# Kernel tuning notes

Hardware: AMD Instinct MI355X
Metric: run time of the kernel (lower is better)

The kernel has to match this reference:

```python
import jax, jax.numpy as jnp
import numpy as np

B, M, D = 512, 100000, 256
EPS = 1e-8  # torch.cosine_similarity eps
TEMP = 10.0  # softmax temperature from source


def setup_inputs() -> dict:
    key = jax.random.key(0)
    kx, kk, kv = jax.random.split(key, 3)
    x = jax.random.normal(kx, (B, D), dtype=jnp.float32)
    memory_keys = jax.random.normal(kk, (M, D), dtype=jnp.float32) * 0.1
    memory_values = jax.random.normal(kv, (M, D), dtype=jnp.float32) * 0.1
    return {"x": x, "memory_keys": memory_keys, "memory_values": memory_values}


def reference(x, memory_keys, memory_values):
    # cosine similarity between x [B,D] and memory_keys [M,D] -> [B,M]
    dots = jnp.einsum("bd,md->bm", x, memory_keys)
    xn = jnp.linalg.norm(x, axis=-1)          # [B]
    kn = jnp.linalg.norm(memory_keys, axis=-1)  # [M]
    denom = jnp.maximum(xn[:, None] * kn[None, :], EPS)
    sims = dots / denom                         # [B,M]
    attn = jax.nn.softmax(sims * TEMP, axis=-1)  # [B,M]
    retrieved = jnp.einsum("bm,md->bd", attn, memory_values)  # [B,D]
    return retrieved, attn
```

## Files before the change

### kernel.cpp

```cpp
#include <hip/hip_runtime.h>
#include <hip/hip_bf16.h>


#define MCOLS 100000
#define MP    100032
#define DDIM  256
#define CHUNK 1792
#define NTFULL 28
#define NCHUNK 56
#define NSLOT 56
#define CHUNK1 832
#define NT1   26
#define ATTN_OFF 131072
#define WS_RXN  0
#define WS_RKN  512
#define WS_RCPL 100512
#define WS_XB_BYTE   409600ull
#define WS_VT_BYTE   1048576ull
#define WS_PART_BYTE 52264960ull
#define WS_KB_BYTE   84246528ull
#define WS_KB_END    (WS_KB_BYTE + 2ull*(size_t)MCOLS*DDIM)

#define GLL(g, l) __builtin_amdgcn_global_load_lds( \
    (const __attribute__((address_space(1))) void*)(g), \
    (__attribute__((address_space(3))) void*)(l), 16, 0, 0)

typedef short short8 __attribute__((ext_vector_type(8)));
typedef float f32x4  __attribute__((ext_vector_type(4)));

static __device__ __forceinline__ unsigned short f2bfu(float f) {
  union { __hip_bfloat16 h; unsigned short u; } cv;
  cv.h = __float2bfloat16(f);
  return cv.u;
}
static __device__ __forceinline__ unsigned int pk2(float a, float b) {
  return (unsigned int)f2bfu(a) | ((unsigned int)f2bfu(b) << 16);
}
static __device__ __forceinline__ short8 pack8(float4 a, float4 b) {
  short8 r;
  r[0] = (short)f2bfu(a.x); r[1] = (short)f2bfu(a.y);
  r[2] = (short)f2bfu(a.z); r[3] = (short)f2bfu(a.w);
  r[4] = (short)f2bfu(b.x); r[5] = (short)f2bfu(b.y);
  r[6] = (short)f2bfu(b.z); r[7] = (short)f2bfu(b.w);
  return r;
}

__global__ void k0_xn(const float* __restrict__ x, float* __restrict__ ws) {
  const int b = blockIdx.x, t = threadIdx.x;
  const float v = x[b*DDIM + t];
  float s = v*v;
  #pragma unroll
  for (int mk = 1; mk <= 32; mk <<= 1) s += __shfl_xor(s, mk);
  __shared__ float ps[4];
  if ((t & 63) == 0) ps[t >> 6] = s;
  __syncthreads();
  const float tot = ps[0] + ps[1] + ps[2] + ps[3];
  const float r10 = 10.0f / fmaxf(sqrtf(tot), 1e-12f);
  if (t == 0) ws[WS_RXN + b] = r10;
  unsigned short* xbp = (unsigned short*)((char*)ws + WS_XB_BYTE);
  xbp[b*DDIM + t] = f2bfu(v * r10);
}

template<bool WRITEKB>
__global__ __launch_bounds__(256) void k0c_kn(const float* __restrict__ K,
                                              float* __restrict__ ws) {
  const int t = threadIdx.x;
  const int mg = blockIdx.x*64 + (t >> 2);
  const int qq = t & 3;
  if (mg >= MCOLS) return;
  const float* kp = K + (size_t)mg*DDIM + 64*qq;
  float4 buf[16];
  float ss = 0.f;
  #pragma unroll
  for (int j = 0; j < 16; ++j) {
    buf[j] = *(const float4*)(kp + 4*j);
    ss += buf[j].x*buf[j].x + buf[j].y*buf[j].y + buf[j].z*buf[j].z + buf[j].w*buf[j].w;
  }
  ss += __shfl_xor(ss, 1); ss += __shfl_xor(ss, 2);
  const float rk = 1.0f / fmaxf(sqrtf(ss), 1e-12f);
  if (qq == 0) ws[WS_RKN + mg] = rk;
  if (WRITEKB) {
    unsigned int* kb = (unsigned int*)((char*)ws + WS_KB_BYTE);
    #pragma unroll
    for (int j = 0; j < 8; ++j) {
      const float4 a = buf[2*j], b2 = buf[2*j+1];
      uint4 u;
      u.x = pk2(a.x*rk, a.y*rk);  u.y = pk2(a.z*rk, a.w*rk);
      u.z = pk2(b2.x*rk, b2.y*rk); u.w = pk2(b2.z*rk, b2.w*rk);
      const int slot = (8*qq + j) ^ (mg & 7);
      *(uint4*)(kb + (size_t)mg*128 + slot*4) = u;
    }
  }
}

__global__ __launch_bounds__(256) void k0b_tr(const float* __restrict__ V,
                                              float* __restrict__ ws) {
  const int t = threadIdx.x;
  const int m0 = blockIdx.x * 64;
  __shared__ float vt_f[64][261];
  #pragma unroll
  for (int i = 0; i < 4; ++i) {
    const int ml = (t >> 4) + 16*i;
    const int mg = m0 + ml;
    #pragma unroll
    for (int j = 0; j < 4; ++j) {
      const int d = 4*(t & 15) + 64*j;
      float4 v = make_float4(0.f, 0.f, 0.f, 0.f);
      if (mg < MCOLS) v = *(const float4*)(V + (size_t)mg*DDIM + d);
      vt_f[ml][d] = v.x; vt_f[ml][d+1] = v.y; vt_f[ml][d+2] = v.z; vt_f[ml][d+3] = v.w;
    }
  }
  __syncthreads();
  unsigned short* vt = (unsigned short*)((char*)ws + WS_VT_BYTE);
  const int tl = t & 15;
  const int s = tl >> 1, hf = tl & 1;
  const int mq = 8*s + 4*hf;
  #pragma unroll
  for (int it = 0; it < 16; ++it) {
    const int d = (t >> 4) + 16*it;
    uint2 u;
    u.x = pk2(vt_f[mq+0][d], vt_f[mq+1][d]);
    u.y = pk2(vt_f[mq+2][d], vt_f[mq+3][d]);
    const int sp = s ^ (d & 7);
    *(uint2*)(vt + (size_t)d*MP + m0 + sp*8 + 4*hf) = u;
  }
}

static __device__ __forceinline__ void stage_k(const char* __restrict__ kb,
                                               int m0, int w, int l,
                                               unsigned short (*klds)[256]) {
  #pragma unroll
  for (int i = 0; i < 4; ++i) {
    int r = m0 + w*8 + i*2 + (l >> 5);
    r = min(r, MCOLS - 1);
    const char* g = kb + (size_t)r*512 + (l & 31)*16;
    char* dst = (char*)&klds[w*8 + i*2][0];
    GLL(g, dst);
  }
}
static __device__ __forceinline__ void stage_k32(const char* __restrict__ kb,
                                                 int m0, int w, int l,
                                                 unsigned short (*klds)[256]) {
  #pragma unroll
  for (int i = 0; i < 2; ++i) {
    int r = m0 + w*4 + i*2 + (l >> 5);
    r = min(r, MCOLS - 1);
    const char* g = kb + (size_t)r*512 + (l & 31)*16;
    char* dst = (char*)&klds[w*4 + i*2][0];
    GLL(g, dst);
  }
}
static __device__ __forceinline__ void stage_vt(const char* __restrict__ vtb,
                                                int m1, int w, int l,
                                                unsigned short (*vtl)[64]) {
  #pragma unroll
  for (int i = 0; i < 4; ++i) {
    const int d = w*32 + i*8 + (l >> 3);
    const int ms = min(m1 + (l & 7)*8, MP - 8);
    const char* g = vtb + ((size_t)d*MP + ms)*2;
    char* dst = (char*)&vtl[w*32 + i*8][0];
    GLL(g, dst);
  }
}

__global__ __launch_bounds__(512, 4) void k1b_sum(const float* __restrict__ ws,
                                                  float* __restrict__ out) {
  const int bid = blockIdx.x;
  const int xg = bid & 7, i = bid >> 3;
  const int c = xg + 8*(i & 15), rb = i >> 4;
  const int t = threadIdx.x, w = t >> 6, l = t & 63, q = l >> 4, ln = l & 15;
  const int ar = w & 3, h = w >> 2, l7 = ln & 7;
  __shared__ __align__(16) unsigned short klds2[2][32][256];
  const char* kb = (const char*)ws + WS_KB_BYTE;
  const unsigned short* xb = (const unsigned short*)((const char*)ws + WS_XB_BYTE);
  const int R0 = rb*128;

  short8 xf[2][8];
  #pragma unroll
  for (int as = 0; as < 2; ++as) {
    const int row = R0 + 32*ar + 16*as + ln;
    #pragma unroll
    for (int kk = 0; kk < 8; ++kk)
      xf[as][kk] = *(const short8*)(xb + row*DDIM + 32*kk + 8*q);
  }
  float lpr[2][4] = {{0.f,0.f,0.f,0.f},{0.f,0.f,0.f,0.f}};
  const int mbase = c*CHUNK1;
  const int rem = MCOLS - mbase;
  const int nt = rem <= 0 ? 0 : min(NT1, (rem + 31) >> 5);

  if (nt > 0) {
    stage_k32(kb, mbase, w, l, klds2[0]);
    __syncthreads();
    for (int mt = 0; mt < nt; ++mt) {
      const int cur = mt & 1;
      const int m0 = mbase + mt*32;
      if (mt + 1 < nt) stage_k32(kb, m0 + 32, w, l, klds2[cur ^ 1]);
      const char* kbase = (const char*)&klds2[cur][0][0];
      const int row0 = 16*h + ln;
      f32x4 acc[2];
      { f32x4 z = {0.f,0.f,0.f,0.f}; acc[0] = z; acc[1] = z; }
      #pragma unroll
      for (int kk = 0; kk < 8; ++kk) {
        const int sl = ((q + 4*kk) ^ l7) << 4;
        const short8 b0 = *(const short8*)(kbase + row0*512 + sl);
        acc[0] = __builtin_amdgcn_mfma_f32_16x16x32_bf16(xf[0][kk], b0, acc[0], 0,0,0);
        acc[1] = __builtin_amdgcn_mfma_f32_16x16x32_bf16(xf[1][kk], b0, acc[1], 0,0,0);
      }
      const int mr = m0 + row0;
      const bool ok = mr < MCOLS;
      #pragma unroll
      for (int as = 0; as < 2; ++as)
        #pragma unroll
        for (int r = 0; r < 4; ++r)
          lpr[as][r] += ok ? __expf(acc[as][r]) : 0.f;
      __syncthreads();
    }
  }
  #pragma unroll
  for (int as = 0; as < 2; ++as)
    #pragma unroll
    for (int r = 0; r < 4; ++r) {
      float s = lpr[as][r];
      s += __shfl_xor(s, 1); s += __shfl_xor(s, 2);
      s += __shfl_xor(s, 4); s += __shfl_xor(s, 8);
      if (ln == 0)
        out[(size_t)(c*2 + h)*512 + R0 + 32*ar + 16*as + 4*q + r] = s;
    }
}

template<int NSUM>
__global__ void k2_final(const float* __restrict__ out, float* __restrict__ ws) {
  const int b = blockIdx.x, t = threadIdx.x;
  float v = (t < NSUM) ? out[(size_t)t*512 + b] : 0.f;
  #pragma unroll
  for (int mk = 1; mk <= 32; mk <<= 1) v += __shfl_xor(v, mk);
  __shared__ float s2[4];
  if ((t & 63) == 0) s2[t >> 6] = v;
  __syncthreads();
  if (t == 0) ws[WS_RCPL + b] = 1.0f / (s2[0] + s2[1] + s2[2] + s2[3]);
}

__global__ __launch_bounds__(512, 4) void k3a_main(float* __restrict__ ws,
                                                   float* __restrict__ out) {
  const int bid = blockIdx.x;
  const int xg = bid & 7, i = bid >> 3;
  const int c = xg + 8*(i % 7), rb = i / 7;
  const int t = threadIdx.x, w = t >> 6, l = t & 63, q = l >> 4, ln = l & 15;
  const int ar = w & 3, h = w >> 2, l7 = ln & 7;
  __shared__ __align__(16) unsigned short klds[64][256];
  __shared__ __align__(16) unsigned short vtl[256][64];
  __shared__ __align__(16) unsigned short plds[64][64];
  const char* kb  = (const char*)ws + WS_KB_BYTE;
  const char* vtb = (const char*)ws + WS_VT_BYTE;
  const unsigned short* xb = (const unsigned short*)((const char*)ws + WS_XB_BYTE);
  const int R0 = rb*64;

  short8 xf[8];
  {
    const int row = R0 + 16*ar + ln;
    #pragma unroll
    for (int kk = 0; kk < 8; ++kk)
      xf[kk] = *(const short8*)(xb + row*DDIM + 32*kk + 8*q);
  }
  float rlq[4];
  #pragma unroll
  for (int r = 0; r < 4; ++r)
    rlq[r] = ws[WS_RCPL + R0 + 16*ar + 4*q + r];
  f32x4 apv[8];
  #pragma unroll
  for (int dx = 0; dx < 8; ++dx) { f32x4 z = {0.f,0.f,0.f,0.f}; apv[dx] = z; }
  const int d2 = 128*h;
  float* attn = out + ATTN_OFF;
  const int mbase = c*CHUNK;
  const int nt = min(NTFULL, (MCOLS - mbase + 63) >> 6);
  unsigned short* pf = &plds[0][0];

  stage_k(kb, mbase, w, l, klds);
  __syncthreads();

  for (int mt = 0; mt < nt; ++mt) {
    const int m0 = mbase + mt*64;
    stage_vt(vtb, m0, w, l, vtl);
    const int row0 = 32*h + ln;
    f32x4 acc[2];
    { f32x4 z = {0.f,0.f,0.f,0.f}; acc[0] = z; acc[1] = z; }
    #pragma unroll
    for (int kk = 0; kk < 8; ++kk) {
      const int sl = ((q + 4*kk) ^ l7) << 4;
      const short8 b0 = *(const short8*)((const char*)&klds[0][0] + row0*512 + sl);
      const short8 b1 = *(const short8*)((const char*)&klds[0][0] + (row0 + 16)*512 + sl);
      acc[0] = __builtin_amdgcn_mfma_f32_16x16x32_bf16(xf[kk], b0, acc[0], 0,0,0);
      acc[1] = __builtin_amdgcn_mfma_f32_16x16x32_bf16(xf[kk], b1, acc[1], 0,0,0);
    }
    const int mr0 = m0 + row0, mr1 = mr0 + 16;
    const bool ok0 = mr0 < MCOLS, ok1 = mr1 < MCOLS;
    #pragma unroll
    for (int r = 0; r < 4; ++r) {
      const int rowl = 16*ar + 4*q + r;
      const float p0v = ok0 ? __expf(acc[0][r]) : 0.f;
      const float p1v = ok1 ? __expf(acc[1][r]) : 0.f;
      float* arow = attn + (size_t)(R0 + rowl)*MCOLS;
      if (ok0) arow[mr0] = p0v*rlq[r];
      if (ok1) arow[mr1] = p1v*rlq[r];
      const int r7 = rowl & 7;
      pf[rowl*64 + ((((ln>>3) + 4*h    ) ^ r7) << 3) + (ln & 7)] = f2bfu(p0v);
      pf[rowl*64 + ((((ln>>3) + 4*h + 2) ^ r7) << 3) + (ln & 7)] = f2bfu(p1v);
    }
    __syncthreads();
    if (mt + 1 < nt) stage_k(kb, m0 + 64, w, l, klds);
    const int prow = 16*ar + ln;
    const short8 af0 = *(const short8*)(pf + prow*64 + ((q       ^ l7) << 3));
    const short8 af1 = *(const short8*)(pf + prow*64 + (((4 + q) ^ l7) << 3));
    #pragma unroll
    for (int dx = 0; dx < 8; ++dx) {
      const int R = d2 + 16*dx + ln;
      const char* vr = (const char*)&vtl[0][0] + R*128;
      const short8 bv0 = *(const short8*)(vr + ((q       ^ l7) << 4));
      const short8 bv1 = *(const short8*)(vr + (((4 + q) ^ l7) << 4));
      apv[dx] = __builtin_amdgcn_mfma_f32_16x16x32_bf16(af0, bv0, apv[dx], 0,0,0);
      apv[dx] = __builtin_amdgcn_mfma_f32_16x16x32_bf16(af1, bv1, apv[dx], 0,0,0);
    }
    __syncthreads();
  }

  float* part = (float*)((char*)ws + WS_PART_BYTE);
  #pragma unroll
  for (int dx = 0; dx < 8; ++dx)
    #pragma unroll
    for (int r = 0; r < 4; ++r)
      part[((size_t)c*512 + R0 + 16*ar + 4*q + r)*256 + d2 + 16*dx + ln]
        = apv[dx][r]*rlq[r];
}

static __device__ __forceinline__ void load_xf(const float* __restrict__ x,
                                               int brow0, int q, int ln,
                                               short8 xf[2][8]) {
  #pragma unroll
  for (int as = 0; as < 2; ++as) {
    const int row = brow0 + 16*as + ln;
    #pragma unroll
    for (int kk = 0; kk < 8; ++kk) {
      const float* p = x + row*DDIM + 32*kk + 8*q;
      xf[as][kk] = pack8(*(const float4*)p, *(const float4*)(p + 4));
    }
  }
}

__global__ __launch_bounds__(512, 2) void k3b_main(const float* __restrict__ x,
                                                   const float* __restrict__ K,
                                                   float* __restrict__ ws,
                                                   float* __restrict__ out) {
  const int bid = blockIdx.x;
  const int c = bid >> 2, rb = bid & 3;
  const int t = threadIdx.x, w = t >> 6, l = t & 63, q = l >> 4, ln = l & 15;
  const int h = w & 1, rg = w >> 1;
  __shared__ __align__(16) unsigned short plds[2][128][72];
  const int R0 = rb*128;
  short8 xf[2][8];
  const int brow0 = R0 + 32*rg;
  load_xf(x, brow0, q, ln, xf);
  float rxn[2][4];
  #pragma unroll
  for (int as = 0; as < 2; ++as)
    #pragma unroll
    for (int r = 0; r < 4; ++r)
      rxn[as][r] = ws[WS_RXN + brow0 + 16*as + 4*q + r];
  float lpr[2][4] = {{0.f,0.f,0.f,0.f},{0.f,0.f,0.f,0.f}};
  f32x4 apv[2][8];
  #pragma unroll
  for (int bs = 0; bs < 2; ++bs)
    #pragma unroll
    for (int dx = 0; dx < 8; ++dx) { f32x4 z = {0.f,0.f,0.f,0.f}; apv[bs][dx] = z; }
  const int b2 = 32*(w & 3), d2 = 128*(w >> 2);
  const unsigned short* vt = (const unsigned short*)((const char*)ws + WS_VT_BYTE);
  const float* rknw = ws + WS_RKN;
  float* attn = out + ATTN_OFF;
  const int mbase = c*CHUNK;
  const int nt = min(NTFULL, (MCOLS - mbase + 63) >> 6);
  const int l7 = ln & 7;

  for (int mt = 0; mt < nt; ++mt) {
    const int m0 = mbase + mt*64;
    const int mr0 = m0 + 32*h + ln, mr1 = mr0 + 16;
    const int kr0 = min(mr0, MCOLS-1), kr1 = min(mr1, MCOLS-1);
    f32x4 acc[2][2];
    #pragma unroll
    for (int as = 0; as < 2; ++as)
      #pragma unroll
      for (int mm = 0; mm < 2; ++mm) { f32x4 z = {0.f,0.f,0.f,0.f}; acc[as][mm] = z; }
    const float* p0 = K + (size_t)kr0*DDIM + 8*q;
    const float* p1 = K + (size_t)kr1*DDIM + 8*q;
    #pragma unroll
    for (int kk = 0; kk < 8; ++kk) {
      const short8 b0 = pack8(*(const float4*)(p0 + 32*kk), *(const float4*)(p0 + 32*kk + 4));
      const short8 b1 = pack8(*(const float4*)(p1 + 32*kk), *(const float4*)(p1 + 32*kk + 4));
      acc[0][0] = __builtin_amdgcn_mfma_f32_16x16x32_bf16(xf[0][kk], b0, acc[0][0], 0,0,0);
      acc[0][1] = __builtin_amdgcn_mfma_f32_16x16x32_bf16(xf[0][kk], b1, acc[0][1], 0,0,0);
      acc[1][0] = __builtin_amdgcn_mfma_f32_16x16x32_bf16(xf[1][kk], b0, acc[1][0], 0,0,0);
      acc[1][1] = __builtin_amdgcn_mfma_f32_16x16x32_bf16(xf[1][kk], b1, acc[1][1], 0,0,0);
    }
    const float rk0 = rknw[kr0], rk1 = rknw[kr1];
    const bool ok0 = mr0 < MCOLS, ok1 = mr1 < MCOLS;
    #pragma unroll
    for (int as = 0; as < 2; ++as)
      #pragma unroll
      for (int r = 0; r < 4; ++r) {
        const int rowl = 32*rg + 16*as + 4*q + r;
        const float p0v = ok0 ? __expf(acc[as][0][r]*rxn[as][r]*rk0) : 0.f;
        const float p1v = ok1 ? __expf(acc[as][1][r]*rxn[as][r]*rk1) : 0.f;
        float* arow = attn + (size_t)(R0 + rowl)*MCOLS;
        if (ok0) arow[mr0] = p0v;
        if (ok1) arow[mr1] = p1v;
        lpr[as][r] += p0v + p1v;
        plds[mt & 1][rowl][32*h + ln]      = f2bfu(p0v);
        plds[mt & 1][rowl][32*h + 16 + ln] = f2bfu(p1v);
      }
    __syncthreads();
    const unsigned short (*pb)[72] = plds[mt & 1];
    const short8 af00 = *(const short8*)&pb[b2 + ln][8*q];
    const short8 af01 = *(const short8*)&pb[b2 + ln][32 + 8*q];
    const short8 af10 = *(const short8*)&pb[b2 + 16 + ln][8*q];
    const short8 af11 = *(const short8*)&pb[b2 + 16 + ln][32 + 8*q];
    #pragma unroll
    for (int dx = 0; dx < 8; ++dx) {
      const int R = d2 + 16*dx + ln;
      const size_t rbase = (size_t)R*MP + m0;
      const short8 bv0 = *(const short8*)(vt + rbase + ((q     ^ (R & 7)) << 3));
      const short8 bv1 = *(const short8*)(vt + rbase + (((4+q) ^ (R & 7)) << 3));
      apv[0][dx] = __builtin_amdgcn_mfma_f32_16x16x32_bf16(af00, bv0, apv[0][dx], 0,0,0);
      apv[0][dx] = __builtin_amdgcn_mfma_f32_16x16x32_bf16(af01, bv1, apv[0][dx], 0,0,0);
      apv[1][dx] = __builtin_amdgcn_mfma_f32_16x16x32_bf16(af10, bv0, apv[1][dx], 0,0,0);
      apv[1][dx] = __builtin_amdgcn_mfma_f32_16x16x32_bf16(af11, bv1, apv[1][dx], 0,0,0);
    }
  }

  #pragma unroll
  for (int as = 0; as < 2; ++as)
    #pragma unroll
    for (int r = 0; r < 4; ++r) {
      float s = lpr[as][r];
      s += __shfl_xor(s, 1); s += __shfl_xor(s, 2);
      s += __shfl_xor(s, 4); s += __shfl_xor(s, 8);
      if (ln == 0)
        out[(size_t)(c*2 + h)*512 + brow0 + 16*as + 4*q + r] = s;
    }
  float* part = (float*)((char*)ws + WS_PART_BYTE);
  #pragma unroll
  for (int bs = 0; bs < 2; ++bs)
    #pragma unroll
    for (int dx = 0; dx < 8; ++dx)
      #pragma unroll
      for (int r = 0; r < 4; ++r)
        part[((size_t)c*512 + R0 + b2 + 16*bs + 4*q + r)*256 + d2 + 16*dx + ln]
          = apv[bs][dx][r];
}

template<bool NORM>
__global__ void k4_red(const float* __restrict__ ws, float* __restrict__ out) {
  const int b = blockIdx.x, t = threadIdx.x;
  const float* part = (const float*)((const char*)ws + WS_PART_BYTE);
  float acc = 0.f;
  for (int cc = 0; cc < NSLOT; ++cc)
    acc += part[((size_t)cc*512 + b)*256 + t];
  if (!NORM) acc *= ws[WS_RCPL + b];
  out[b*DDIM + t] = acc;
}

__global__ void k5_scale(const float* __restrict__ ws, float* __restrict__ out) {
  const int row = blockIdx.y;
  const int i4 = blockIdx.x*256 + threadIdx.x;
  if (i4 >= MCOLS/4) return;
  const float s = ws[WS_RCPL + row];
  float4* p = (float4*)(out + ATTN_OFF + (size_t)row*MCOLS) + i4;
  float4 v = *p;
  v.x *= s; v.y *= s; v.z *= s; v.w *= s;
  *p = v;
}

extern "C" void kernel_launch(void* const* d_in, const int* in_sizes, int n_in,
                              void* d_out, int out_size, void* d_ws, size_t ws_size,
                              hipStream_t stream) {
  const float* x = (const float*)d_in[0];
  const float* K = (const float*)d_in[1];
  const float* V = (const float*)d_in[2];
  float* out = (float*)d_out;
  float* ws  = (float*)d_ws;
  const bool useKB = ws_size >= WS_KB_END;

  k0_xn<<<512, 256, 0, stream>>>(x, ws);
  if (useKB) k0c_kn<true ><<<1563, 256, 0, stream>>>(K, ws);
  else       k0c_kn<false><<<1563, 256, 0, stream>>>(K, ws);
  k0b_tr<<<MP/64, 256, 0, stream>>>(V, ws);
  if (useKB) {
    k1b_sum<<<512, 512, 0, stream>>>(ws, out);
    k2_final<256><<<512, 256, 0, stream>>>(out, ws);
    k3a_main<<<448, 512, 0, stream>>>(ws, out);
    k4_red<true><<<512, 256, 0, stream>>>(ws, out);
  } else {
    k3b_main<<<224, 512, 0, stream>>>(x, K, ws, out);
    k2_final<112><<<512, 256, 0, stream>>>(out, ws);
    k5_scale<<<dim3((MCOLS/4 + 255)/256, 512), 256, 0, stream>>>(ws, out);
    k4_red<false><<<512, 256, 0, stream>>>(ws, out);
  }
}
```

Measured before the change: 244.5 us.

## Re-tile k3a warp mapping so each K fragment feeds two x-row tiles

Reassigns warps in k3a_main so each warp owns 32 query rows by 16 memory columns in the QK^T stage, reusing one K LDS fragment across two MFMAs. In the PV stage each warp covers 32 rows by 64 output columns, reusing V fragments across two row tiles. The aim is to halve LDS reads per MFMA. The 1/sum scaling of partial outputs moves out of k3a, and the reduction kernel is switched to the variant that applies it. The cost is more registers for the doubled x fragments.

```diff
diff --git a/kernel.cpp b/kernel.cpp
--- a/kernel.cpp
+++ b/kernel.cpp
@@ -243,10 +243,12 @@
 __global__ __launch_bounds__(512, 4) void k3a_main(float* __restrict__ ws,
                                                    float* __restrict__ out) {
   const int bid = blockIdx.x;
-  const int xg = bid & 7, i = bid >> 3;
-  const int c = xg + 8*(i % 7), rb = i / 7;
+  const int xcd = bid & 7, i = bid >> 3;
+  const int c = xcd + 8*(i % 7), rb = i / 7;
   const int t = threadIdx.x, w = t >> 6, l = t & 63, q = l >> 4, ln = l & 15;
-  const int ar = w & 3, h = w >> 2, l7 = ln & 7;
+  const int l7 = ln & 7;
+  const int xg = w >> 2, mh = w & 3;
+  const int pg = w & 1,  dg = w >> 1;
   __shared__ __align__(16) unsigned short klds[64][256];
   __shared__ __align__(16) unsigned short vtl[256][64];
   __shared__ __align__(16) unsigned short plds[64][64];
@@ -255,21 +257,23 @@
   const unsigned short* xb = (const unsigned short*)((const char*)ws + WS_XB_BYTE);
   const int R0 = rb*64;
 
-  short8 xf[8];
-  {
-    const int row = R0 + 16*ar + ln;
+  short8 xf[2][8];
+  #pragma unroll
+  for (int s = 0; s < 2; ++s) {
+    const int row = R0 + 32*xg + 16*s + ln;
     #pragma unroll
     for (int kk = 0; kk < 8; ++kk)
-      xf[kk] = *(const short8*)(xb + row*DDIM + 32*kk + 8*q);
-  }
-  float rlq[4];
-  #pragma unroll
-  for (int r = 0; r < 4; ++r)
-    rlq[r] = ws[WS_RCPL + R0 + 16*ar + 4*q + r];
+      xf[s][kk] = *(const short8*)(xb + row*DDIM + 32*kk + 8*q);
+  }
+  float rlq[2][4];
+  #pragma unroll
+  for (int s = 0; s < 2; ++s)
+    #pragma unroll
+    for (int r = 0; r < 4; ++r)
+      rlq[s][r] = ws[WS_RCPL + R0 + 32*xg + 16*s + 4*q + r];
   f32x4 apv[8];
   #pragma unroll
   for (int dx = 0; dx < 8; ++dx) { f32x4 z = {0.f,0.f,0.f,0.f}; apv[dx] = z; }
-  const int d2 = 128*h;
   float* attn = out + ATTN_OFF;
   const int mbase = c*CHUNK;
   const int nt = min(NTFULL, (MCOLS - mbase + 63) >> 6);
@@ -281,55 +285,60 @@
   for (int mt = 0; mt < nt; ++mt) {
     const int m0 = mbase + mt*64;
     stage_vt(vtb, m0, w, l, vtl);
-    const int row0 = 32*h + ln;
+    const int brow = 16*mh + ln;
     f32x4 acc[2];
     { f32x4 z = {0.f,0.f,0.f,0.f}; acc[0] = z; acc[1] = z; }
     #pragma unroll
     for (int kk = 0; kk < 8; ++kk) {
-      const int sl = ((q + 4*kk) ^ l7) << 4;
-      const short8 b0 = *(const short8*)((const char*)&klds[0][0] + row0*512 + sl);
-      const short8 b1 = *(const short8*)((const char*)&klds[0][0] + (row0 + 16)*512 + sl);
-      acc[0] = __builtin_amdgcn_mfma_f32_16x16x32_bf16(xf[kk], b0, acc[0], 0,0,0);
-      acc[1] = __builtin_amdgcn_mfma_f32_16x16x32_bf16(xf[kk], b1, acc[1], 0,0,0);
-    }
-    const int mr0 = m0 + row0, mr1 = mr0 + 16;
-    const bool ok0 = mr0 < MCOLS, ok1 = mr1 < MCOLS;
-    #pragma unroll
-    for (int r = 0; r < 4; ++r) {
-      const int rowl = 16*ar + 4*q + r;
-      const float p0v = ok0 ? __expf(acc[0][r]) : 0.f;
-      const float p1v = ok1 ? __expf(acc[1][r]) : 0.f;
-      float* arow = attn + (size_t)(R0 + rowl)*MCOLS;
-      if (ok0) arow[mr0] = p0v*rlq[r];
-      if (ok1) arow[mr1] = p1v*rlq[r];
-      const int r7 = rowl & 7;
-      pf[rowl*64 + ((((ln>>3) + 4*h    ) ^ r7) << 3) + (ln & 7)] = f2bfu(p0v);
-      pf[rowl*64 + ((((ln>>3) + 4*h + 2) ^ r7) << 3) + (ln & 7)] = f2bfu(p1v);
-    }
+      const short8 b0 = *(const short8*)((const char*)&klds[0][0]
+                                         + brow*512 + (((q + 4*kk) ^ l7) << 4));
+      acc[0] = __builtin_amdgcn_mfma_f32_16x16x32_bf16(xf[0][kk], b0, acc[0], 0,0,0);
+      acc[1] = __builtin_amdgcn_mfma_f32_16x16x32_bf16(xf[1][kk], b0, acc[1], 0,0,0);
+    }
+    const int mc = m0 + 16*mh + ln;
+    const bool okc = mc < MCOLS;
+    const int psl = 2*mh + (ln >> 3);
+    #pragma unroll
+    for (int s = 0; s < 2; ++s)
+      #pragma unroll
+      for (int r = 0; r < 4; ++r) {
+        const int rowl = 32*xg + 16*s + 4*q + r;
+        const float p = okc ? __expf(acc[s][r]) : 0.f;
+        if (okc) attn[(size_t)(R0 + rowl)*MCOLS + mc] = p*rlq[s][r];
+        pf[rowl*64 + ((psl ^ (rowl & 7)) << 3) + (ln & 7)] = f2bfu(p);
+      }
     __syncthreads();
     if (mt + 1 < nt) stage_k(kb, m0 + 64, w, l, klds);
-    const int prow = 16*ar + ln;
-    const short8 af0 = *(const short8*)(pf + prow*64 + ((q       ^ l7) << 3));
-    const short8 af1 = *(const short8*)(pf + prow*64 + (((4 + q) ^ l7) << 3));
-    #pragma unroll
-    for (int dx = 0; dx < 8; ++dx) {
-      const int R = d2 + 16*dx + ln;
+    const int pr0 = 32*pg + ln, pr1 = pr0 + 16;
+    const short8 af00 = *(const short8*)(pf + pr0*64 + ((q       ^ l7) << 3));
+    const short8 af01 = *(const short8*)(pf + pr0*64 + (((4 + q) ^ l7) << 3));
+    const short8 af10 = *(const short8*)(pf + pr1*64 + ((q       ^ l7) << 3));
+    const short8 af11 = *(const short8*)(pf + pr1*64 + (((4 + q) ^ l7) << 3));
+    #pragma unroll
+    for (int dx = 0; dx < 4; ++dx) {
+      const int R = 64*dg + 16*dx + ln;
       const char* vr = (const char*)&vtl[0][0] + R*128;
       const short8 bv0 = *(const short8*)(vr + ((q       ^ l7) << 4));
       const short8 bv1 = *(const short8*)(vr + (((4 + q) ^ l7) << 4));
-      apv[dx] = __builtin_amdgcn_mfma_f32_16x16x32_bf16(af0, bv0, apv[dx], 0,0,0);
-      apv[dx] = __builtin_amdgcn_mfma_f32_16x16x32_bf16(af1, bv1, apv[dx], 0,0,0);
+      apv[dx]     = __builtin_amdgcn_mfma_f32_16x16x32_bf16(af00, bv0, apv[dx],     0,0,0);
+      apv[dx]     = __builtin_amdgcn_mfma_f32_16x16x32_bf16(af01, bv1, apv[dx],     0,0,0);
+      apv[4 + dx] = __builtin_amdgcn_mfma_f32_16x16x32_bf16(af10, bv0, apv[4 + dx], 0,0,0);
+      apv[4 + dx] = __builtin_amdgcn_mfma_f32_16x16x32_bf16(af11, bv1, apv[4 + dx], 0,0,0);
     }
     __syncthreads();
   }
 
   float* part = (float*)((char*)ws + WS_PART_BYTE);
   #pragma unroll
-  for (int dx = 0; dx < 8; ++dx)
-    #pragma unroll
-    for (int r = 0; r < 4; ++r)
-      part[((size_t)c*512 + R0 + 16*ar + 4*q + r)*256 + d2 + 16*dx + ln]
-        = apv[dx][r]*rlq[r];
+  for (int st = 0; st < 2; ++st)
+    #pragma unroll
+    for (int dx = 0; dx < 4; ++dx)
+      #pragma unroll
+      for (int r = 0; r < 4; ++r) {
+        const int row = R0 + 32*pg + 16*st + 4*q + r;
+        const int dcol = 64*dg + 16*dx + ln;
+        part[((size_t)c*512 + row)*256 + dcol] = apv[st*4 + dx][r];
+      }
 }
 
 static __device__ __forceinline__ void load_xf(const float* __restrict__ x,
@@ -495,7 +504,7 @@
     k1b_sum<<<512, 512, 0, stream>>>(ws, out);
     k2_final<256><<<512, 256, 0, stream>>>(out, ws);
     k3a_main<<<448, 512, 0, stream>>>(ws, out);
-    k4_red<true><<<512, 256, 0, stream>>>(ws, out);
+    k4_red<false><<<512, 256, 0, stream>>>(ws, out);
   } else {
     k3b_main<<<224, 512, 0, stream>>>(x, K, ws, out);
     k2_final<112><<<512, 256, 0, stream>>>(out, ws);
```

New measurement: 427.6 us. 1.75x slower.
